# Kernel optimization log

Measured on AMD Instinct MI355X. Metric: run time of the kernel, lower is better.

## Reference

```python
import jax, jax.numpy as jnp
import numpy as np

CUTOFF = 5.0
N_PER_L = (20, 18, 16, 14)   # radial features per angular channel l (max_radial=20, Laplacian-eigenstate style taper)
M_PER_L = (1, 3, 5, 7)       # 2l+1
N_ATOMS = 10000
N_EDGES = 200000
N_SPECIES = 100
PSEUDO = 4

_FREQS = np.concatenate([np.arange(1, nl + 1) for nl in N_PER_L]).astype(np.float32)  # [sum(N_PER_L)]


def _radial(r):
    # r: [P] -> [P, sum(N_PER_L)]. Sine (spherical Laplacian eigenstate style) basis with smooth cosine cutoff.
    rc = jnp.clip(r, 0.0, CUTOFF)
    fc = 0.5 * (jnp.cos(jnp.pi * rc / CUTOFF) + 1.0)            # [P]
    return jnp.sin(jnp.asarray(_FREQS) * (jnp.pi / CUTOFF) * r[:, None]) * fc[:, None]


def _angular(R, r):
    # real spherical harmonics up to l=3, [P, 16], ordered l-major (m = -l..l)
    u = R / (r[:, None] + 1e-12)
    x, y, z = u[:, 0], u[:, 1], u[:, 2]
    x2, y2, z2 = x * x, y * y, z * z
    cols = [
        jnp.full_like(x, 0.28209479177387814),
        0.4886025119029199 * y, 0.4886025119029199 * z, 0.4886025119029199 * x,
        1.0925484305920792 * x * y, 1.0925484305920792 * y * z,
        0.31539156525252005 * (3.0 * z2 - 1.0),
        1.0925484305920792 * x * z, 0.5462742152960396 * (x2 - y2),
        0.5900435899266435 * y * (3.0 * x2 - y2), 2.890611442640554 * x * y * z,
        0.4570457994644658 * y * (5.0 * z2 - 1.0), 0.3731763325901154 * z * (5.0 * z2 - 3.0),
        0.4570457994644658 * x * (5.0 * z2 - 1.0), 1.445305721320277 * z * (x2 - y2),
        0.5900435899266435 * x * (x2 - 3.0 * y2),
    ]
    return jnp.stack(cols, axis=-1)


def setup_inputs() -> dict:
    key = jax.random.key(0)
    k1, k2, k3, k4, k5 = jax.random.split(key, 5)
    return {
        "R_ij": jax.random.normal(k1, (N_EDGES, 3), dtype=jnp.float32) * 1.5,
        "i": jnp.sort(jax.random.randint(k2, (N_EDGES,), 0, N_ATOMS)),
        "j": jax.random.randint(k3, (N_EDGES,), 0, N_ATOMS),
        "species": jax.random.randint(k4, (N_ATOMS,), 0, N_SPECIES),
        "species_embed": jax.random.normal(k5, (N_SPECIES, PSEUDO), dtype=jnp.float32),
    }


def reference(R_ij, i, j, species, species_embed):
    r = jnp.sqrt(jnp.sum(R_ij * R_ij, axis=-1))          # [P]
    radial = _radial(r)                                   # [P, sum n_l]
    angular = _angular(R_ij, r)                           # [P, 16]
    sp = species_embed[species[j]]                        # alchemical species channels, [P, 4]
    outs = []
    off_n = 0
    off_m = 0
    for nl, ml in zip(N_PER_L, M_PER_L):
        rl = radial[:, off_n:off_n + nl]                  # [P, n_l]
        al = angular[:, off_m:off_m + ml]                 # [P, 2l+1]
        e = jnp.einsum('pn,pm,pc->pmnc', rl, al, sp)      # fused outer product per edge
        outs.append(jax.ops.segment_sum(e, i, num_segments=N_ATOMS))  # [n_atoms, 2l+1, n_l, 4]
        off_n += nl
        off_m += ml
    return tuple(outs)
```

## Files before the change

### kernel.cpp

```cpp
#include <hip/hip_runtime.h>

#define N_ATOMS 10000
#define N_EDGES 200000
#define GA 4
#define EB 128
#define ROW 44
#define W_F 0.6283185307179586f

__global__ __launch_bounds__(256) void seg_starts_kernel(
    const int* __restrict__ seg_i, int* __restrict__ starts)
{
    const int a = blockIdx.x * blockDim.x + threadIdx.x;
    if (a > N_ATOMS) return;
    int lo = 0, hi = N_EDGES;
    while (lo < hi) {
        int mid = (lo + hi) >> 1;
        if (seg_i[mid] < a) lo = mid + 1; else hi = mid;
    }
    starts[a] = lo;
}

__global__ __launch_bounds__(256) void sph_expand_kernel(
    const float* __restrict__ R,
    const int*   __restrict__ starts,
    const int*   __restrict__ idx_j,
    const int*   __restrict__ species,
    const float* __restrict__ emb,
    float*       __restrict__ out)
{
    __shared__ float feat[EB][ROW];
    const int tid  = threadIdx.x;
    const int wave = tid >> 6;
    const int lane = tid & 63;
    const int atom_base = blockIdx.x * GA;
    const int atom = atom_base + wave;

    int n0 = 0, m0 = 0, m1 = 0, nl = 0, pidx = 0, stride = 0; long base = 0;
    const bool active = (lane < 43);
    if (lane < 5)        { n0 = 4*lane;                                   m0 = 0; m1 = 0;                        nl = 20; pidx = 0;       base = 0;       stride = 80;  }
    else if (lane < 15)  { int q = lane-5;  int pr = q/5;  n0 = 4*(q%5);  m0 = 2*pr; m1 = (m0+1 < 3) ? m0+1 : 2; nl = 18; pidx = 1 + pr;  base = 800000;  stride = 216; }
    else if (lane < 27)  { int q = lane-15; int pr = q/4;  n0 = 4*(q%4);  m0 = 2*pr; m1 = (m0+1 < 5) ? m0+1 : 4; nl = 16; pidx = 3 + pr;  base = 2960000; stride = 320; }
    else if (lane < 43)  { int q = lane-27; int pr = q/4;  n0 = 4*(q%4);  m0 = 2*pr; m1 = (m0+1 < 7) ? m0+1 : 6; nl = 14; pidx = 6 + pr;  base = 6160000; stride = 392; }

    float4 acc[8];
    #pragma unroll
    for (int k = 0; k < 8; ++k) acc[k] = float4{0.f, 0.f, 0.f, 0.f};

    const int gstart = starts[atom_base];
    const int gend   = starts[atom_base + GA];
    const int astart = starts[atom];
    const int aend   = starts[atom + 1];

    for (int e0 = gstart; e0 < gend; e0 += EB) {
        const int cnt = min(EB, gend - e0);
        __syncthreads();
        if (tid < cnt) {
            const int g = e0 + tid;
            const int jj = idx_j[g];
            const float x = R[3*g + 0];
            const float y = R[3*g + 1];
            const float z = R[3*g + 2];
            const int sidx = species[jj];
            const float r   = sqrtf(x*x + y*y + z*z);
            const float inv = 1.0f / (r + 1e-12f);
            const float ux = x*inv, uy = y*inv, uz = z*inv;
            const float4 spv = *(const float4*)&emb[4 * sidx];

            const float t1 = W_F * r;
            const float s1 = sinf(t1);
            const float c1 = cosf(t1);
            const float fc = (r < 5.0f) ? (0.5f * (c1 + 1.0f)) : 0.0f;
            const float c2x = 2.0f * c1;

            float rb[20];
            {
                float sk_2 = 0.0f, sk_1 = s1;
                rb[0] = s1 * fc;
                #pragma unroll
                for (int k = 1; k < 20; ++k) {
                    const float sk = c2x * sk_1 - sk_2;
                    rb[k] = sk * fc;
                    sk_2 = sk_1; sk_1 = sk;
                }
            }

            const float x2 = ux*ux, y2 = uy*uy, z2 = uz*uz;
            const float c1a = 0.4886025119029199f;
            const float c2a = 1.0925484305920792f;
            float an[16];
            an[0]  = 0.28209479177387814f;
            an[1]  = c1a * uy;
            an[2]  = c1a * uz;
            an[3]  = c1a * ux;
            an[4]  = c2a * ux * uy;
            an[5]  = c2a * uy * uz;
            an[6]  = 0.31539156525252005f * (3.0f*z2 - 1.0f);
            an[7]  = c2a * ux * uz;
            an[8]  = 0.5462742152960396f * (x2 - y2);
            an[9]  = 0.5900435899266435f * uy * (3.0f*x2 - y2);
            an[10] = 2.890611442640554f  * ux * uy * uz;
            an[11] = 0.4570457994644658f * uy * (5.0f*z2 - 1.0f);
            an[12] = 0.3731763325901154f * uz * (5.0f*z2 - 3.0f);
            an[13] = 0.4570457994644658f * ux * (5.0f*z2 - 1.0f);
            an[14] = 1.445305721320277f  * uz * (x2 - y2);
            an[15] = 0.5900435899266435f * ux * (x2 - 3.0f*y2);

            float4* row = (float4*)&feat[tid][0];
            row[0]  = float4{rb[0],  rb[1],  rb[2],  rb[3]};
            row[1]  = float4{rb[4],  rb[5],  rb[6],  rb[7]};
            row[2]  = float4{rb[8],  rb[9],  rb[10], rb[11]};
            row[3]  = float4{rb[12], rb[13], rb[14], rb[15]};
            row[4]  = float4{rb[16], rb[17], rb[18], rb[19]};
            row[5]  = float4{an[0],  an[0],  an[1],  an[2]};
            row[6]  = float4{an[3],  an[3],  an[4],  an[5]};
            row[7]  = float4{an[6],  an[7],  an[8],  an[8]};
            row[8]  = float4{an[9],  an[10], an[11], an[12]};
            row[9]  = float4{an[13], an[14], an[15], an[15]};
            row[10] = spv;
        }
        __syncthreads();

        const int lo = max(astart, e0);
        const int hi = min(aend, e0 + cnt);
        if (active) {
            for (int e = lo; e < hi; ++e) {
                const float* f = &feat[e - e0][0];
                const float4 rq = *(const float4*)(f + n0);
                const float2 ap = *(const float2*)(f + 20 + 2*pidx);
                const float4 sv = *(const float4*)(f + 40);
                const float rr[4] = {rq.x, rq.y, rq.z, rq.w};
                const float aa[2] = {ap.x, ap.y};
                #pragma unroll
                for (int mi = 0; mi < 2; ++mi) {
                    #pragma unroll
                    for (int ni = 0; ni < 4; ++ni) {
                        const float p = rr[ni] * aa[mi];
                        float4& A = acc[mi*4 + ni];
                        A.x += p * sv.x; A.y += p * sv.y; A.z += p * sv.z; A.w += p * sv.w;
                    }
                }
            }
        }
    }

    if (active) {
        float* ob = out + base + (size_t)atom * (size_t)stride;
        #pragma unroll
        for (int mi = 0; mi < 2; ++mi) {
            if (mi == 0 || m1 != m0) {
                const int m = mi ? m1 : m0;
                #pragma unroll
                for (int ni = 0; ni < 4; ++ni) {
                    const int n = n0 + ni;
                    if (n < nl) *(float4*)(ob + (size_t)(m*nl + n)*4) = acc[mi*4 + ni];
                }
            }
        }
    }
}

extern "C" void kernel_launch(void* const* d_in, const int* in_sizes, int n_in,
                              void* d_out, int out_size, void* d_ws, size_t ws_size,
                              hipStream_t stream) {
    const float* R    = (const float*)d_in[0];
    const int*   i_   = (const int*)  d_in[1];
    const int*   j_   = (const int*)  d_in[2];
    const int*   sp   = (const int*)  d_in[3];
    const float* emb  = (const float*)d_in[4];
    float* out = (float*)d_out;
    int*   starts = (int*)d_ws;

    seg_starts_kernel<<<(N_ATOMS + 256) / 256, 256, 0, stream>>>(i_, starts);
    sph_expand_kernel<<<N_ATOMS / GA, 256, 0, stream>>>(R, starts, j_, sp, emb, out);
}
```

Before: 96.66 us.

## Use one wave per atom and fold segment search into the main kernel

Drops the separate segment-start kernel. Each single-wave block now finds its own atom's edge range with a windowed binary search near atom*20, then a ballot scan for the end. Featurisation is done only for the atom's own edges in 56-edge chunks, with wave barriers replacing block-wide syncs. This removes a kernel launch, the redundant group-wide edge staging and block syncs, at the cost of more small blocks and some per-block search overhead.

New measurement: 95.26 us. About the same (-1.4%).

```diff
diff --git a/kernel.cpp b/kernel.cpp
--- a/kernel.cpp
+++ b/kernel.cpp
@@ -2,38 +2,44 @@
 
 #define N_ATOMS 10000
 #define N_EDGES 200000
-#define GA 4
-#define EB 128
+#define EB 56
 #define ROW 44
 #define W_F 0.6283185307179586f
 
-__global__ __launch_bounds__(256) void seg_starts_kernel(
-    const int* __restrict__ seg_i, int* __restrict__ starts)
-{
-    const int a = blockIdx.x * blockDim.x + threadIdx.x;
-    if (a > N_ATOMS) return;
-    int lo = 0, hi = N_EDGES;
-    while (lo < hi) {
-        int mid = (lo + hi) >> 1;
-        if (seg_i[mid] < a) lo = mid + 1; else hi = mid;
-    }
-    starts[a] = lo;
-}
-
-__global__ __launch_bounds__(256) void sph_expand_kernel(
+__global__ __launch_bounds__(64, 4) void sph_kernel(
     const float* __restrict__ R,
-    const int*   __restrict__ starts,
+    const int*   __restrict__ seg_i,
     const int*   __restrict__ idx_j,
     const int*   __restrict__ species,
     const float* __restrict__ emb,
     float*       __restrict__ out)
 {
     __shared__ float feat[EB][ROW];
-    const int tid  = threadIdx.x;
-    const int wave = tid >> 6;
-    const int lane = tid & 63;
-    const int atom_base = blockIdx.x * GA;
-    const int atom = atom_base + wave;
+    const int atom = blockIdx.x;
+    const int lane = threadIdx.x;
+
+    int lo = 0, hi = N_EDGES;
+    {
+        const int g = atom * 20;
+        int wlo = g - 2048; if (wlo < 0) wlo = 0;
+        int whi = g + 2048; if (whi > N_EDGES) whi = N_EDGES;
+        const bool ok_lo = (wlo == 0)       || (seg_i[wlo - 1] < atom);
+        const bool ok_hi = (whi == N_EDGES) || (seg_i[whi] >= atom);
+        if (ok_lo && ok_hi) { lo = wlo; hi = whi; }
+    }
+    while (lo < hi) {
+        int mid = (lo + hi) >> 1;
+        if (seg_i[mid] < atom) lo = mid + 1; else hi = mid;
+    }
+    const int s = lo;
+    int e = s;
+    for (;;) {
+        const int probe = e + lane;
+        const int v = (probe < N_EDGES) ? seg_i[probe] : (N_ATOMS + 1);
+        const unsigned long long m = __ballot(v > atom);
+        if (m) { e += __ffsll((long long)m) - 1; break; }
+        e += 64;
+    }
 
     int n0 = 0, m0 = 0, m1 = 0, nl = 0, pidx = 0, stride = 0; long base = 0;
     const bool active = (lane < 43);
@@ -46,16 +52,11 @@
     #pragma unroll
     for (int k = 0; k < 8; ++k) acc[k] = float4{0.f, 0.f, 0.f, 0.f};
 
-    const int gstart = starts[atom_base];
-    const int gend   = starts[atom_base + GA];
-    const int astart = starts[atom];
-    const int aend   = starts[atom + 1];
+    for (int e0 = s; e0 < e; e0 += EB) {
+        const int cnt = min(EB, e - e0);
 
-    for (int e0 = gstart; e0 < gend; e0 += EB) {
-        const int cnt = min(EB, gend - e0);
-        __syncthreads();
-        if (tid < cnt) {
-            const int g = e0 + tid;
+        if (lane < cnt) {
+            const int g = e0 + lane;
             const int jj = idx_j[g];
             const float x = R[3*g + 0];
             const float y = R[3*g + 1];
@@ -105,7 +106,7 @@
             an[14] = 1.445305721320277f  * uz * (x2 - y2);
             an[15] = 0.5900435899266435f * ux * (x2 - 3.0f*y2);
 
-            float4* row = (float4*)&feat[tid][0];
+            float4* row = (float4*)&feat[lane][0];
             row[0]  = float4{rb[0],  rb[1],  rb[2],  rb[3]};
             row[1]  = float4{rb[4],  rb[5],  rb[6],  rb[7]};
             row[2]  = float4{rb[8],  rb[9],  rb[10], rb[11]};
@@ -118,13 +119,11 @@
             row[9]  = float4{an[13], an[14], an[15], an[15]};
             row[10] = spv;
         }
-        __syncthreads();
+        __builtin_amdgcn_wave_barrier();
 
-        const int lo = max(astart, e0);
-        const int hi = min(aend, e0 + cnt);
         if (active) {
-            for (int e = lo; e < hi; ++e) {
-                const float* f = &feat[e - e0][0];
+            const float* f = &feat[0][0];
+            for (int t = 0; t < cnt; ++t, f += ROW) {
                 const float4 rq = *(const float4*)(f + n0);
                 const float2 ap = *(const float2*)(f + 20 + 2*pidx);
                 const float4 sv = *(const float4*)(f + 40);
@@ -141,6 +140,7 @@
                 }
             }
         }
+        __builtin_amdgcn_wave_barrier();
     }
 
     if (active) {
@@ -168,8 +168,6 @@
     const int*   sp   = (const int*)  d_in[3];
     const float* emb  = (const float*)d_in[4];
     float* out = (float*)d_out;
-    int*   starts = (int*)d_ws;
 
-    seg_starts_kernel<<<(N_ATOMS + 256) / 256, 256, 0, stream>>>(i_, starts);
-    sph_expand_kernel<<<N_ATOMS / GA, 256, 0, stream>>>(R, starts, j_, sp, emb, out);
+    sph_kernel<<<N_ATOMS, 64, 0, stream>>>(R, i_, j_, sp, emb, out);
 }
```

## Fuse segment search into expansion kernel with producer/consumer wave split

Applied to the files above, without the earlier changes.

Removes the separate segment-start kernel. Each block now finds its own segment boundaries with a wave-cooperative 64-way search, narrowed by a window guess of about 20 edges per atom. Blocks now cover 2 atoms, with two producer waves computing edge features into shared memory and two consumer waves accumulating. Launch bounds request higher occupancy. This saves a launch and the global round trip for the starts, at the cost of redundant searches in every block and only half the waves doing accumulation.

Result: slower. 121.8 us (+26.0%).

```diff
diff --git a/kernel.cpp b/kernel.cpp
--- a/kernel.cpp
+++ b/kernel.cpp
@@ -2,27 +2,39 @@
 
 #define N_ATOMS 10000
 #define N_EDGES 200000
-#define GA 4
-#define EB 128
+#define GA 2
+#define EB 112
 #define ROW 44
 #define W_F 0.6283185307179586f
 
-__global__ __launch_bounds__(256) void seg_starts_kernel(
-    const int* __restrict__ seg_i, int* __restrict__ starts)
-{
-    const int a = blockIdx.x * blockDim.x + threadIdx.x;
-    if (a > N_ATOMS) return;
-    int lo = 0, hi = N_EDGES;
+__device__ __forceinline__ int lb64(const int* __restrict__ a, int lo, int hi, int v, int lane) {
     while (lo < hi) {
-        int mid = (lo + hi) >> 1;
-        if (seg_i[mid] < a) lo = mid + 1; else hi = mid;
+        const int len  = hi - lo;
+        const int step = (len + 63) >> 6;
+        const int p    = lo + lane * step;
+        const unsigned long long m = __ballot((p < hi) && (a[p] < v));
+        const int nb = __popcll(m);
+        if (nb == 0) { hi = lo; break; }
+        const int lastlt = lo + (nb - 1) * step;
+        lo = lastlt + 1;
+        hi = min(lastlt + step, hi);
     }
-    starts[a] = lo;
+    return lo;
 }
 
-__global__ __launch_bounds__(256) void sph_expand_kernel(
+__device__ __forceinline__ int seg_lb(const int* __restrict__ a, int v, int lane) {
+    int lo = 0, hi = N_EDGES;
+    const int est = 20 * v;
+    int wlo = est - 2048; if (wlo < 0) wlo = 0;
+    int whi = est + 2048; if (whi > N_EDGES) whi = N_EDGES;
+    const bool ok = ((wlo == 0) || (a[wlo - 1] < v)) && ((whi == N_EDGES) || (a[whi] >= v));
+    if (ok) { lo = wlo; hi = whi; }
+    return lb64(a, lo, hi, v, lane);
+}
+
+__global__ __launch_bounds__(256, 8) void sph_kernel(
     const float* __restrict__ R,
-    const int*   __restrict__ starts,
+    const int*   __restrict__ seg_i,
     const int*   __restrict__ idx_j,
     const int*   __restrict__ species,
     const float* __restrict__ emb,
@@ -32,99 +44,83 @@
     const int tid  = threadIdx.x;
     const int wave = tid >> 6;
     const int lane = tid & 63;
-    const int atom_base = blockIdx.x * GA;
-    const int atom = atom_base + wave;
+    const int gb   = blockIdx.x * GA;
+
+    const int s0 = seg_lb(seg_i, gb,     lane);
+    const int s1 = seg_lb(seg_i, gb + 1, lane);
+    const int s2 = seg_lb(seg_i, gb + 2, lane);
 
     int n0 = 0, m0 = 0, m1 = 0, nl = 0, pidx = 0, stride = 0; long base = 0;
-    const bool active = (lane < 43);
     if (lane < 5)        { n0 = 4*lane;                                   m0 = 0; m1 = 0;                        nl = 20; pidx = 0;       base = 0;       stride = 80;  }
     else if (lane < 15)  { int q = lane-5;  int pr = q/5;  n0 = 4*(q%5);  m0 = 2*pr; m1 = (m0+1 < 3) ? m0+1 : 2; nl = 18; pidx = 1 + pr;  base = 800000;  stride = 216; }
     else if (lane < 27)  { int q = lane-15; int pr = q/4;  n0 = 4*(q%4);  m0 = 2*pr; m1 = (m0+1 < 5) ? m0+1 : 4; nl = 16; pidx = 3 + pr;  base = 2960000; stride = 320; }
     else if (lane < 43)  { int q = lane-27; int pr = q/4;  n0 = 4*(q%4);  m0 = 2*pr; m1 = (m0+1 < 7) ? m0+1 : 6; nl = 14; pidx = 6 + pr;  base = 6160000; stride = 392; }
+    const bool consumer = (wave >= 2);
+    const bool racc     = consumer && (lane < 43);
+    const int  atom     = gb + (wave - 2);
+    const int  astart   = (wave == 2) ? s0 : s1;
+    const int  aend     = (wave == 2) ? s1 : s2;
 
     float4 acc[8];
     #pragma unroll
     for (int k = 0; k < 8; ++k) acc[k] = float4{0.f, 0.f, 0.f, 0.f};
 
-    const int gstart = starts[atom_base];
-    const int gend   = starts[atom_base + GA];
-    const int astart = starts[atom];
-    const int aend   = starts[atom + 1];
+    for (int e0 = s0; e0 < s2; e0 += EB) {
+        const int cnt = min(EB, s2 - e0);
+        __syncthreads();
+        if (tid < 128) {
+            for (int t = tid; t < cnt; t += 128) {
+                const int g = e0 + t;
+                const int jj = idx_j[g];
+                const float x = R[3*g + 0];
+                const float y = R[3*g + 1];
+                const float z = R[3*g + 2];
+                const int sidx = species[jj];
+                const float r   = sqrtf(x*x + y*y + z*z);
+                const float inv = 1.0f / (r + 1e-12f);
+                const float ux = x*inv, uy = y*inv, uz = z*inv;
+                const float4 spv = *(const float4*)&emb[4 * sidx];
 
-    for (int e0 = gstart; e0 < gend; e0 += EB) {
-        const int cnt = min(EB, gend - e0);
-        __syncthreads();
-        if (tid < cnt) {
-            const int g = e0 + tid;
-            const int jj = idx_j[g];
-            const float x = R[3*g + 0];
-            const float y = R[3*g + 1];
-            const float z = R[3*g + 2];
-            const int sidx = species[jj];
-            const float r   = sqrtf(x*x + y*y + z*z);
-            const float inv = 1.0f / (r + 1e-12f);
-            const float ux = x*inv, uy = y*inv, uz = z*inv;
-            const float4 spv = *(const float4*)&emb[4 * sidx];
+                const float t1 = W_F * r;
+                const float s1f = sinf(t1);
+                const float c1f = cosf(t1);
+                const float fc  = (r < 5.0f) ? (0.5f * (c1f + 1.0f)) : 0.0f;
+                const float c2x = 2.0f * c1f;
 
-            const float t1 = W_F * r;
-            const float s1 = sinf(t1);
-            const float c1 = cosf(t1);
-            const float fc = (r < 5.0f) ? (0.5f * (c1 + 1.0f)) : 0.0f;
-            const float c2x = 2.0f * c1;
-
-            float rb[20];
-            {
-                float sk_2 = 0.0f, sk_1 = s1;
-                rb[0] = s1 * fc;
-                #pragma unroll
-                for (int k = 1; k < 20; ++k) {
-                    const float sk = c2x * sk_1 - sk_2;
-                    rb[k] = sk * fc;
-                    sk_2 = sk_1; sk_1 = sk;
+                float4* row = (float4*)&feat[t][0];
+                {
+                    float sk_2 = 0.0f, sk_1 = s1f;
+                    #pragma unroll
+                    for (int qd = 0; qd < 5; ++qd) {
+                        float q0, q1, q2, q3;
+                        if (qd == 0) { q0 = s1f; }
+                        else { const float sk = c2x*sk_1 - sk_2; sk_2 = sk_1; sk_1 = sk; q0 = sk; }
+                        { const float sk = c2x*sk_1 - sk_2; sk_2 = sk_1; sk_1 = sk; q1 = sk; }
+                        { const float sk = c2x*sk_1 - sk_2; sk_2 = sk_1; sk_1 = sk; q2 = sk; }
+                        { const float sk = c2x*sk_1 - sk_2; sk_2 = sk_1; sk_1 = sk; q3 = sk; }
+                        row[qd] = float4{q0*fc, q1*fc, q2*fc, q3*fc};
+                    }
                 }
+                const float x2 = ux*ux, y2 = uy*uy, z2 = uz*uz;
+                const float c1a = 0.4886025119029199f;
+                const float c2a = 1.0925484305920792f;
+                row[5] = float4{0.28209479177387814f, 0.28209479177387814f, c1a*uy, c1a*uz};
+                row[6] = float4{c1a*ux, c1a*ux, c2a*ux*uy, c2a*uy*uz};
+                row[7] = float4{0.31539156525252005f*(3.0f*z2-1.0f), c2a*ux*uz,
+                                0.5462742152960396f*(x2-y2), 0.5462742152960396f*(x2-y2)};
+                row[8] = float4{0.5900435899266435f*uy*(3.0f*x2-y2), 2.890611442640554f*ux*uy*uz,
+                                0.4570457994644658f*uy*(5.0f*z2-1.0f), 0.3731763325901154f*uz*(5.0f*z2-3.0f)};
+                row[9] = float4{0.4570457994644658f*ux*(5.0f*z2-1.0f), 1.445305721320277f*uz*(x2-y2),
+                                0.5900435899266435f*ux*(x2-3.0f*y2), 0.5900435899266435f*ux*(x2-3.0f*y2)};
+                row[10] = spv;
             }
-
-            const float x2 = ux*ux, y2 = uy*uy, z2 = uz*uz;
-            const float c1a = 0.4886025119029199f;
-            const float c2a = 1.0925484305920792f;
-            float an[16];
-            an[0]  = 0.28209479177387814f;
-            an[1]  = c1a * uy;
-            an[2]  = c1a * uz;
-            an[3]  = c1a * ux;
-            an[4]  = c2a * ux * uy;
-            an[5]  = c2a * uy * uz;
-            an[6]  = 0.31539156525252005f * (3.0f*z2 - 1.0f);
-            an[7]  = c2a * ux * uz;
-            an[8]  = 0.5462742152960396f * (x2 - y2);
-            an[9]  = 0.5900435899266435f * uy * (3.0f*x2 - y2);
-            an[10] = 2.890611442640554f  * ux * uy * uz;
-            an[11] = 0.4570457994644658f * uy * (5.0f*z2 - 1.0f);
-            an[12] = 0.3731763325901154f * uz * (5.0f*z2 - 3.0f);
-            an[13] = 0.4570457994644658f * ux * (5.0f*z2 - 1.0f);
-            an[14] = 1.445305721320277f  * uz * (x2 - y2);
-            an[15] = 0.5900435899266435f * ux * (x2 - 3.0f*y2);
-
-            float4* row = (float4*)&feat[tid][0];
-            row[0]  = float4{rb[0],  rb[1],  rb[2],  rb[3]};
-            row[1]  = float4{rb[4],  rb[5],  rb[6],  rb[7]};
-            row[2]  = float4{rb[8],  rb[9],  rb[10], rb[11]};
-            row[3]  = float4{rb[12], rb[13], rb[14], rb[15]};
-            row[4]  = float4{rb[16], rb[17], rb[18], rb[19]};
-            row[5]  = float4{an[0],  an[0],  an[1],  an[2]};
-            row[6]  = float4{an[3],  an[3],  an[4],  an[5]};
-            row[7]  = float4{an[6],  an[7],  an[8],  an[8]};
-            row[8]  = float4{an[9],  an[10], an[11], an[12]};
-            row[9]  = float4{an[13], an[14], an[15], an[15]};
-            row[10] = spv;
         }
         __syncthreads();
-
-        const int lo = max(astart, e0);
-        const int hi = min(aend, e0 + cnt);
-        if (active) {
-            for (int e = lo; e < hi; ++e) {
-                const float* f = &feat[e - e0][0];
+        if (racc) {
+            const int lo = max(astart, e0);
+            const int hi = min(aend, e0 + cnt);
+            const float* f = &feat[lo - e0][0];
+            for (int t = lo; t < hi; ++t, f += ROW) {
                 const float4 rq = *(const float4*)(f + n0);
                 const float2 ap = *(const float2*)(f + 20 + 2*pidx);
                 const float4 sv = *(const float4*)(f + 40);
@@ -143,7 +139,7 @@
         }
     }
 
-    if (active) {
+    if (racc) {
         float* ob = out + base + (size_t)atom * (size_t)stride;
         #pragma unroll
         for (int mi = 0; mi < 2; ++mi) {
@@ -168,8 +164,6 @@
     const int*   sp   = (const int*)  d_in[3];
     const float* emb  = (const float*)d_in[4];
     float* out = (float*)d_out;
-    int*   starts = (int*)d_ws;
 
-    seg_starts_kernel<<<(N_ATOMS + 256) / 256, 256, 0, stream>>>(i_, starts);
-    sph_expand_kernel<<<N_ATOMS / GA, 256, 0, stream>>>(R, starts, j_, sp, emb, out);
+    sph_kernel<<<N_ATOMS / GA, 256, 0, stream>>>(R, i_, j_, sp, emb, out);
 }
```
